# Kernel tuning notes

Hardware: AMD Instinct MI355X
Metric: run time of the kernel (lower is better)

## Reference

```python
import jax, jax.numpy as jnp
import numpy as np

N, D, E = 50000, 128, 100000
H1, H2, H3 = 8, 8, 4
NEG_SLOPE = 0.2  # PyG GATv2Conv default negative_slope


def _gatv2_layer(x, src, dst, Wl, Wr, att, b, heads):
    # GATv2Conv(in=D, out=D, heads=heads, concat=False), share_weights=False
    C = Wl.shape[1] // heads
    xl = (x @ Wl).reshape(-1, heads, C)  # source-side transform (x_j)
    xr = (x @ Wr).reshape(-1, heads, C)  # target-side transform (x_i)
    m = jax.nn.leaky_relu(xl[src] + xr[dst], NEG_SLOPE)      # [E,H,C]
    e = jnp.einsum('ehc,hc->eh', m, att)                      # [E,H]
    # segment softmax over incoming edges of each destination node
    emax = jax.ops.segment_max(e, dst, num_segments=N)        # [N,H]
    a = jnp.exp(e - emax[dst])
    denom = jax.ops.segment_sum(a, dst, num_segments=N)       # [N,H] (>0: self-loops)
    a = a / denom[dst]
    out = jax.ops.segment_sum(xl[src] * a[:, :, None], dst, num_segments=N)  # [N,H,C]
    return out.mean(axis=1) + b  # concat=False -> head mean, then bias


def setup_inputs() -> dict:
    key = jax.random.key(0)
    ks = jax.random.split(key, 16)
    x = jax.random.normal(ks[0], (N, D), dtype=jnp.float32)
    src = jax.random.randint(ks[1], (E,), 0, N)
    dst = jax.random.randint(ks[2], (E,), 0, N)
    src = jnp.where(src == dst, (src + 1) % N, src)  # no pre-existing self loops
    edge_index = jnp.stack([src, dst]).astype(jnp.int64)
    s = 1.0 / np.sqrt(D)
    def lin(k, h):
        return jax.random.uniform(k, (D, h * D), jnp.float32, -s, s)
    def attn(k, h):
        return jax.random.uniform(k, (h, D), jnp.float32, -s, s)
    return {
        'x': x, 'edge_index': edge_index,
        'W1l': lin(ks[3], H1), 'W1r': lin(ks[4], H1), 'att1': attn(ks[5], H1), 'b1': jnp.zeros((D,), jnp.float32),
        'W2l': lin(ks[6], H2), 'W2r': lin(ks[7], H2), 'att2': attn(ks[8], H2), 'b2': jnp.zeros((D,), jnp.float32),
        'W3l': lin(ks[9], H3), 'W3r': lin(ks[10], H3), 'att3': attn(ks[11], H3), 'b3': jnp.zeros((D,), jnp.float32),
    }


def reference(x, edge_index, W1l, W1r, att1, b1, W2l, W2r, att2, b2, W3l, W3r, att3, b3):
    # PyG GATv2Conv adds self loops by default
    loops = jnp.arange(N, dtype=edge_index.dtype)
    src = jnp.concatenate([edge_index[0], loops])
    dst = jnp.concatenate([edge_index[1], loops])
    h = x + _gatv2_layer(x, src, dst, W1l, W1r, att1, b1, H1)
    h = jax.nn.elu(h)  # dropout is identity in eval mode
    h = h + _gatv2_layer(h, src, dst, W2l, W2r, att2, b2, H2)
    h = jax.nn.elu(h)
    h = h + _gatv2_layer(h, src, dst, W3l, W3r, att3, b3, H3)
    return h
```

## Files before the change

kernel.cpp:

```cpp
#include <hip/hip_runtime.h>

#define NN 50000
#define DD 128
#define EE 100000
#define ET (EE + NN)

typedef __attribute__((ext_vector_type(4))) float f32x4;
typedef __attribute__((ext_vector_type(8))) short bf16x8;
typedef __attribute__((ext_vector_type(4))) unsigned short u16x4;
typedef __attribute__((ext_vector_type(4))) unsigned int u32x4;
typedef __attribute__((ext_vector_type(2))) unsigned int u32x2;

static __device__ __forceinline__ unsigned short f2bf(float f) {
  union { float f; unsigned int u; } v; v.f = f;
  unsigned int r = (v.u + 0x7FFFu + ((v.u >> 16) & 1u)) >> 16;
  return (unsigned short)r;
}
static __device__ __forceinline__ float bflo(unsigned int u) {
  union { unsigned int u; float f; } v; v.u = u << 16; return v.f;
}
static __device__ __forceinline__ float bfhi(unsigned int u) {
  union { unsigned int u; float f; } v; v.u = u & 0xffff0000u; return v.f;
}

template <int CTRL>
static __device__ __forceinline__ float dpp_add(float x) {
  int xi = __builtin_bit_cast(int, x);
  int yi = __builtin_amdgcn_update_dpp(xi, xi, CTRL, 0xF, 0xF, true);
  return x + __builtin_bit_cast(float, yi);
}
static __device__ __forceinline__ float row16_sum(float p) {
  p = dpp_add<0xB1>(p);
  p = dpp_add<0x4E>(p);
  p = dpp_add<0x141>(p);
  p = dpp_add<0x128>(p);
  return p;
}

__global__ __launch_bounds__(256) void k_prep(
    const float* __restrict__ x, const int* __restrict__ ei,
    const float* __restrict__ W1l, const float* __restrict__ W1r,
    const float* __restrict__ W2l, const float* __restrict__ W2r,
    const float* __restrict__ W3l, const float* __restrict__ W3r,
    const float* __restrict__ att1, const float* __restrict__ att2, const float* __restrict__ att3,
    unsigned short* __restrict__ wt1, unsigned short* __restrict__ wt2,
    unsigned short* __restrict__ wt3,
    float* __restrict__ as1, float* __restrict__ as2, float* __restrict__ as3,
    unsigned short* __restrict__ abf, int* __restrict__ counts) {
  const int i = blockIdx.x * 256 + threadIdx.x;
  const float LOG2E = 1.4426950408889634f;
  if (i < 262144) {
    int half = i >> 17, rem = i & 131071;
    int nn = rem >> 7, k = rem & 127;
    const float* W = half ? W1r : W1l;
    wt1[i] = f2bf(W[(size_t)k * 1024 + nn]);
  } else if (i < 524288) {
    int local = i - 262144;
    int half = local >> 17, rem = local & 131071;
    int nn = rem >> 7, k = rem & 127;
    const float* W = half ? W2r : W2l;
    wt2[local] = f2bf(W[(size_t)k * 1024 + nn]);
  } else if (i < 655360) {
    int local = i - 524288;
    int half = local >> 16, rem = local & 65535;
    int nn = rem >> 7, k = rem & 127;
    const float* W = half ? W3r : W3l;
    wt3[local] = f2bf(W[(size_t)k * 512 + nn]);
  } else if (i < 657920) {
    int local = i - 655360;
    if (local < 1024) as1[local] = att1[local] * LOG2E;
    else if (local < 2048) as2[local - 1024] = att2[local - 1024] * LOG2E;
    else as3[local - 2048] = att3[local - 2048] * LOG2E;
  } else if (i < 807920) {
    int e = i - 657920;
    int dst = (e < EE) ? ei[EE + e] : (e - EE);
    if (dst >= 0 && dst < NN) atomicAdd(&counts[dst], 1);
  } else if (i < 2407920) {
    int u = i - 807920;
    f32x4 v = *(const f32x4*)(x + (size_t)u * 4);
    u16x4 w;
    w.x = f2bf(v.x); w.y = f2bf(v.y); w.z = f2bf(v.z); w.w = f2bf(v.w);
    *(u16x4*)(abf + (size_t)u * 4) = w;
  }
}

__global__ __launch_bounds__(1024) void k_scan(const int* __restrict__ counts,
                                               int* __restrict__ offs,
                                               int* __restrict__ cursor) {
  __shared__ int wsum[16];
  __shared__ int wpre[16];
  __shared__ int wtot;
  const int tid = threadIdx.x;
  const int wv = tid >> 6, lane = tid & 63;
  int carry = 0;
  for (int base = 0; base < NN; base += 4096) {
    int i0 = base + tid * 4;
    int v[4];
#pragma unroll
    for (int q = 0; q < 4; ++q) { int i = i0 + q; v[q] = (i < NN) ? counts[i] : 0; }
    int s = v[0] + v[1] + v[2] + v[3];
    int sc = s;
#pragma unroll
    for (int m = 1; m < 64; m <<= 1) {
      int t = __shfl_up(sc, m, 64);
      if (lane >= m) sc += t;
    }
    if (lane == 63) wsum[wv] = sc;
    __syncthreads();
    if (tid < 16) {
      int t = wsum[tid];
      int scc = t;
#pragma unroll
      for (int m = 1; m < 16; m <<= 1) {
        int u = __shfl_up(scc, m, 64);
        if (tid >= m) scc += u;
      }
      wpre[tid] = scc - t;
      if (tid == 15) wtot = scc;
    }
    __syncthreads();
    int excl = carry + wpre[wv] + (sc - s);
#pragma unroll
    for (int q = 0; q < 4; ++q) {
      int i = i0 + q;
      if (i < NN) { offs[i] = excl; cursor[i] = excl; }
      excl += v[q];
    }
    carry += wtot;
    __syncthreads();
  }
  if (tid == 0) offs[NN] = carry;
}

__global__ void k_fill(const int* __restrict__ ei, int* __restrict__ cursor,
                       int* __restrict__ srcs) {
  int i = blockIdx.x * blockDim.x + threadIdx.x;
  if (i >= ET) return;
  int src, dst;
  if (i < EE) { src = ei[i]; dst = ei[EE + i]; }
  else { src = dst = i - EE; }
  if (dst < 0 || dst >= NN) return;
  if (src < 0 || src >= NN) src = dst;
  int pos = atomicAdd(&cursor[dst], 1);
  if (pos >= 0 && pos < ET) srcs[pos] = src;
}

__global__ __launch_bounds__(256) void gemm_bt(
    const unsigned short* __restrict__ A, const unsigned short* __restrict__ WT,
    unsigned short* __restrict__ Cl, unsigned short* __restrict__ Cr,
    int M, int Nout, int lgny) {
  const int f = (blockIdx.x & 7) * (gridDim.x >> 3) + (blockIdx.x >> 3);
  const int c = f & ((1 << lgny) - 1);
  const int x = f >> lgny;
  const int z = c & 1, y = c >> 1;
  const int m0 = x * 128, n0 = y * 128;
  unsigned short* C = z ? Cr : Cl;
  const unsigned short* BT = WT + (size_t)z * Nout * DD;

  __shared__ unsigned short As[128 * 128];
  __shared__ unsigned short Bs[128 * 128];
  const int tid = threadIdx.x;
  const int wave = tid >> 6, lane = tid & 63;
  const int hi = lane >> 4, lr = lane & 15;

#pragma unroll
  for (int i = 0; i < 8; ++i) {
    int row = i * 16 + wave * 4 + hi;
    int c16 = lr ^ (row & 7);
    const unsigned short* ga = A + (size_t)(m0 + row) * DD + c16 * 8;
    __builtin_amdgcn_global_load_lds((const __attribute__((address_space(1))) void*)ga,
        (__attribute__((address_space(3))) void*)(As + i * 2048 + wave * 512), 16, 0, 0);
    const unsigned short* gb = BT + (size_t)(n0 + row) * DD + c16 * 8;
    __builtin_amdgcn_global_load_lds((const __attribute__((address_space(1))) void*)gb,
        (__attribute__((address_space(3))) void*)(Bs + i * 2048 + wave * 512), 16, 0, 0);
  }
  __syncthreads();

  const int wr = (wave >> 1) * 64, wc = (wave & 1) * 64;
  f32x4 acc[4][4];
#pragma unroll
  for (int i = 0; i < 4; ++i)
#pragma unroll
    for (int j = 0; j < 4; ++j) acc[i][j] = (f32x4){0.f, 0.f, 0.f, 0.f};

#pragma unroll
  for (int k0 = 0; k0 < 128; k0 += 32) {
    const int ck = (k0 >> 3) + hi;
    bf16x8 af[4], bfr[4];
#pragma unroll
    for (int mi = 0; mi < 4; ++mi) {
      int r = wr + mi * 16 + lr;
      af[mi] = *(const bf16x8*)&As[r * 128 + ((ck ^ (r & 7)) << 3)];
    }
#pragma unroll
    for (int ni = 0; ni < 4; ++ni) {
      int cc = wc + ni * 16 + lr;
      bfr[ni] = *(const bf16x8*)&Bs[cc * 128 + ((ck ^ (cc & 7)) << 3)];
    }
#pragma unroll
    for (int mi = 0; mi < 4; ++mi)
#pragma unroll
      for (int ni = 0; ni < 4; ++ni)
        acc[mi][ni] = __builtin_amdgcn_mfma_f32_16x16x32_bf16(af[mi], bfr[ni], acc[mi][ni], 0, 0, 0);
  }

#pragma unroll
  for (int mi = 0; mi < 4; ++mi) {
#pragma unroll
    for (int ni = 0; ni < 4; ++ni) {
      int col = n0 + wc + ni * 16 + lr;
#pragma unroll
      for (int j = 0; j < 4; ++j) {
        int row = m0 + wr + mi * 16 + (hi << 2) + j;
        if (row < M) C[(size_t)row * Nout + col] = f2bf(acc[mi][ni][j]);
      }
    }
  }
}

template <int H>
__global__ __launch_bounds__(256) void gat_agg8(
    const unsigned short* __restrict__ xl, const unsigned short* __restrict__ xr,
    const int* __restrict__ offs, const int* __restrict__ srcs,
    const float* __restrict__ att_s,
    const float* __restrict__ bias,
    const float* __restrict__ residf,
    const unsigned short* __restrict__ residb,
    float* __restrict__ outf,
    unsigned short* __restrict__ hbfw,
    int do_elu) {
  constexpr int HG = H / 2;
  constexpr int CPL = 2 * HG;
  constexpr int NW = HG;
  constexpr int LPH = 128 / CPL;
  constexpr int ROW = H * DD;
  constexpr int HALFROW = ROW / 2;
  const int wave = threadIdx.x >> 6, lane = threadIdx.x & 63;
  const int nsub = wave >> 1, g = wave & 1;
  const int n = blockIdx.x * 2 + nsub;
  if (n >= NN) return;
  const int cb = g * HALFROW + lane * CPL;
  const int d0 = (lane * CPL) & 127;

  float xrv[CPL], av[CPL];
  {
    unsigned int uw[NW];
    if constexpr (NW == 4) {
      u32x4 v = *(const u32x4*)(xr + (size_t)n * ROW + cb);
      uw[0] = v.x; uw[1] = v.y; uw[2] = v.z; uw[3] = v.w;
    } else {
      u32x2 v = *(const u32x2*)(xr + (size_t)n * ROW + cb);
      uw[0] = v.x; uw[1] = v.y;
    }
#pragma unroll
    for (int w = 0; w < NW; ++w) {
      xrv[2 * w] = bflo(uw[w]);
      xrv[2 * w + 1] = bfhi(uw[w]);
    }
#pragma unroll
    for (int c = 0; c < CPL; ++c) av[c] = att_s[cb + c];
  }

  float acc[CPL];
#pragma unroll
  for (int c = 0; c < CPL; ++c) acc[c] = 0.f;
  float mx = -1e30f, dn = 0.f;

  const int e0 = offs[n], e1 = offs[n + 1];
  const unsigned short* xl_cb = xl + cb;
  for (int j = e0; j < e1; j += 4) {
    const int B = (e1 - j < 4) ? (e1 - j) : 4;
    unsigned int rows[4][NW];
#pragma unroll
    for (int b = 0; b < 4; ++b) {
      if (b < B) {
        int s = srcs[j + b];
        if constexpr (NW == 4) {
          u32x4 v = *(const u32x4*)(xl_cb + (size_t)s * ROW);
          rows[b][0] = v.x; rows[b][1] = v.y; rows[b][2] = v.z; rows[b][3] = v.w;
        } else {
          u32x2 v = *(const u32x2*)(xl_cb + (size_t)s * ROW);
          rows[b][0] = v.x; rows[b][1] = v.y;
        }
      }
    }
    float p[4];
#pragma unroll
    for (int b = 0; b < 4; ++b) {
      float pp = -1e30f;
      if (b < B) {
        pp = 0.f;
#pragma unroll
        for (int w = 0; w < NW; ++w) {
          float x0 = bflo(rows[b][w]), x1 = bfhi(rows[b][w]);
          float z0 = x0 + xrv[2 * w]; z0 = fmaxf(z0, 0.2f * z0);
          float z1 = x1 + xrv[2 * w + 1]; z1 = fmaxf(z1, 0.2f * z1);
          pp = fmaf(z0, av[2 * w], pp);
          pp = fmaf(z1, av[2 * w + 1], pp);
        }
        pp = row16_sum(pp);
        if constexpr (LPH == 32) pp += __shfl_xor(pp, 16, 64);
      }
      p[b] = pp;
    }
    float pm = fmaxf(fmaxf(p[0], p[1]), fmaxf(p[2], p[3]));
    if (__any(pm > mx + 11.5f)) {
      float mnew = fmaxf(mx, pm);
      float sc = __builtin_amdgcn_exp2f(mx - mnew);
      dn *= sc;
#pragma unroll
      for (int c = 0; c < CPL; ++c) acc[c] *= sc;
      mx = mnew;
    }
#pragma unroll
    for (int b = 0; b < 4; ++b) {
      if (b < B) {
        float wt = __builtin_amdgcn_exp2f(p[b] - mx);
        dn += wt;
#pragma unroll
        for (int w = 0; w < NW; ++w) {
          acc[2 * w] = fmaf(wt, bflo(rows[b][w]), acc[2 * w]);
          acc[2 * w + 1] = fmaf(wt, bfhi(rows[b][w]), acc[2 * w + 1]);
        }
      }
    }
  }

  float r[CPL];
  const float inv = (1.f / (float)H) / dn;
#pragma unroll
  for (int c = 0; c < CPL; ++c) r[c] = acc[c] * inv;
#pragma unroll
  for (int m = LPH; m < 64; m <<= 1)
#pragma unroll
    for (int c = 0; c < CPL; ++c) r[c] += __shfl_xor(r[c], m, 64);

  __shared__ float lds[2][DD];
  if (g == 1 && lane < LPH) {
#pragma unroll
    for (int c = 0; c < CPL; ++c) lds[nsub][d0 + c] = r[c];
  }
  __syncthreads();
  if (g == 0 && lane < LPH) {
    float rv[CPL];
    if (residf) {
#pragma unroll
      for (int c = 0; c < CPL; c += 4) {
        f32x4 v = *(const f32x4*)(residf + (size_t)n * DD + d0 + c);
        rv[c] = v.x; rv[c + 1] = v.y; rv[c + 2] = v.z; rv[c + 3] = v.w;
      }
    } else {
      unsigned int uw[CPL / 2];
      if constexpr (CPL == 8) {
        u32x4 v = *(const u32x4*)(residb + (size_t)n * DD + d0);
        uw[0] = v.x; uw[1] = v.y; uw[2] = v.z; uw[3] = v.w;
      } else {
        u32x2 v = *(const u32x2*)(residb + (size_t)n * DD + d0);
        uw[0] = v.x; uw[1] = v.y;
      }
#pragma unroll
      for (int w = 0; w < CPL / 2; ++w) {
        rv[2 * w] = bflo(uw[w]);
        rv[2 * w + 1] = bfhi(uw[w]);
      }
    }
    float o[CPL];
#pragma unroll
    for (int c = 0; c < CPL; ++c) {
      o[c] = r[c] + lds[nsub][d0 + c] + bias[d0 + c] + rv[c];
      if (do_elu && o[c] < 0.f)
        o[c] = __builtin_amdgcn_exp2f(o[c] * 1.4426950408889634f) - 1.f;
    }
    if (outf) {
#pragma unroll
      for (int c = 0; c < CPL; c += 4) {
        f32x4 v; v.x = o[c]; v.y = o[c + 1]; v.z = o[c + 2]; v.w = o[c + 3];
        *(f32x4*)(outf + (size_t)n * DD + d0 + c) = v;
      }
    }
    if (hbfw) {
      unsigned int pk[CPL / 2];
#pragma unroll
      for (int q = 0; q < CPL / 2; ++q)
        pk[q] = (unsigned int)f2bf(o[2 * q]) | ((unsigned int)f2bf(o[2 * q + 1]) << 16);
      if constexpr (CPL == 8) {
        u32x4 v; v.x = pk[0]; v.y = pk[1]; v.z = pk[2]; v.w = pk[3];
        *(u32x4*)(hbfw + (size_t)n * DD + d0) = v;
      } else {
        u32x2 v; v.x = pk[0]; v.y = pk[1];
        *(u32x2*)(hbfw + (size_t)n * DD + d0) = v;
      }
    }
  }
}

extern "C" void kernel_launch(void* const* d_in, const int* in_sizes, int n_in,
                              void* d_out, int out_size, void* d_ws, size_t ws_size,
                              hipStream_t stream) {
  const float* x = (const float*)d_in[0];
  const int* ei = (const int*)d_in[1];
  const float* W1l = (const float*)d_in[2];
  const float* W1r = (const float*)d_in[3];
  const float* att1 = (const float*)d_in[4];
  const float* b1 = (const float*)d_in[5];
  const float* W2l = (const float*)d_in[6];
  const float* W2r = (const float*)d_in[7];
  const float* att2 = (const float*)d_in[8];
  const float* b2 = (const float*)d_in[9];
  const float* W3l = (const float*)d_in[10];
  const float* W3r = (const float*)d_in[11];
  const float* att3 = (const float*)d_in[12];
  const float* b3 = (const float*)d_in[13];
  float* out = (float*)d_out;

  char* p = (char*)d_ws;
  auto carve = [&](size_t bytes) {
    char* r = p;
    p += (bytes + 255) & ~(size_t)255;
    return r;
  };
  unsigned short* xl = (unsigned short*)carve((size_t)NN * 1024 * 2);
  unsigned short* xr = (unsigned short*)carve((size_t)NN * 1024 * 2);
  unsigned short* abf = (unsigned short*)carve((size_t)NN * DD * 2);
  unsigned short* wt1 = (unsigned short*)carve((size_t)2 * 1024 * DD * 2);
  unsigned short* wt2 = (unsigned short*)carve((size_t)2 * 1024 * DD * 2);
  unsigned short* wt3 = (unsigned short*)carve((size_t)2 * 512 * DD * 2);
  float* as1 = (float*)carve((size_t)8 * DD * 4);
  float* as2 = (float*)carve((size_t)8 * DD * 4);
  float* as3 = (float*)carve((size_t)4 * DD * 4);
  int* counts = (int*)carve((size_t)NN * 4);
  int* offs = (int*)carve(((size_t)NN + 1) * 4);
  int* cursor = (int*)carve((size_t)NN * 4);
  int* srcs = (int*)carve((size_t)ET * 4);
  size_t needed = (size_t)(p - (char*)d_ws);
  if (needed > ws_size) return;

  hipMemsetAsync(counts, 0, (size_t)NN * 4, stream);
  k_prep<<<9406, 256, 0, stream>>>(x, ei, W1l, W1r, W2l, W2r, W3l, W3r, att1, att2, att3,
                                   wt1, wt2, wt3, as1, as2, as3, abf, counts);
  k_scan<<<1, 1024, 0, stream>>>(counts, offs, cursor);
  k_fill<<<(ET + 255) / 256, 256, 0, stream>>>(ei, cursor, srcs);

  const int gx = (NN + 127) / 128;
  const int ga = (NN + 1) / 2;
  gemm_bt<<<gx * 16, 256, 0, stream>>>(abf, wt1, xl, xr, NN, 1024, 4);
  gat_agg8<8><<<ga, 256, 0, stream>>>(xl, xr, offs, srcs, as1, b1, x, nullptr,
                                      nullptr, abf, 1);
  gemm_bt<<<gx * 16, 256, 0, stream>>>(abf, wt2, xl, xr, NN, 1024, 4);
  gat_agg8<8><<<ga, 256, 0, stream>>>(xl, xr, offs, srcs, as2, b2, nullptr, abf,
                                      nullptr, abf, 1);
  gemm_bt<<<gx * 8, 256, 0, stream>>>(abf, wt3, xl, xr, NN, 512, 3);
  gat_agg8<4><<<ga, 256, 0, stream>>>(xl, xr, offs, srcs, as3, b3, nullptr, abf,
                                      out, nullptr, 0);
}
```

Baseline: 451.9 us.

## Shrink GEMM tiles to 64x64 and transpose weights via LDS-tiled kernel

Replaces the 128x128 bf16 MFMA GEMM tile with a 64x64 tile, launching more blocks with a quarter of the LDS each to improve occupancy and load balance. Moves the weight transpose/convert out of the elementwise prep kernel into a dedicated kernel that stages 64x64 tiles in shared memory for coalesced reads and writes. Smaller tiles reduce operand reuse, increasing global traffic for A and W.

```diff
diff --git a/kernel.cpp b/kernel.cpp
--- a/kernel.cpp
+++ b/kernel.cpp
@@ -37,46 +37,59 @@
   return p;
 }
 
-__global__ __launch_bounds__(256) void k_prep(
-    const float* __restrict__ x, const int* __restrict__ ei,
+__global__ __launch_bounds__(256) void k_wtr(
     const float* __restrict__ W1l, const float* __restrict__ W1r,
     const float* __restrict__ W2l, const float* __restrict__ W2r,
     const float* __restrict__ W3l, const float* __restrict__ W3r,
+    unsigned short* __restrict__ wt1, unsigned short* __restrict__ wt2,
+    unsigned short* __restrict__ wt3) {
+  __shared__ float t[64][65];
+  int b = blockIdx.x;
+  const float* W; unsigned short* WT; int Nout, lgn;
+  int half, tile;
+  if (b < 64) {
+    half = b >> 5; tile = b & 31; W = half ? W1r : W1l;
+    WT = wt1 + (size_t)half * 131072; Nout = 1024; lgn = 4;
+  } else if (b < 128) {
+    b -= 64; half = b >> 5; tile = b & 31; W = half ? W2r : W2l;
+    WT = wt2 + (size_t)half * 131072; Nout = 1024; lgn = 4;
+  } else {
+    b -= 128; half = b >> 4; tile = b & 15; W = half ? W3r : W3l;
+    WT = wt3 + (size_t)half * 65536; Nout = 512; lgn = 3;
+  }
+  const int k0 = (tile >> lgn) << 6;
+  const int n0 = (tile & ((1 << lgn) - 1)) << 6;
+  const int wv = threadIdx.x >> 6, ln = threadIdx.x & 63;
+#pragma unroll
+  for (int r = 0; r < 16; ++r) {
+    int row = r * 4 + wv;
+    t[row][ln] = W[(size_t)(k0 + row) * Nout + n0 + ln];
+  }
+  __syncthreads();
+#pragma unroll
+  for (int r = 0; r < 16; ++r) {
+    int nrow = r * 4 + wv;
+    WT[(size_t)(n0 + nrow) * 128 + k0 + ln] = f2bf(t[ln][nrow]);
+  }
+}
+
+__global__ __launch_bounds__(256) void k_prep(
+    const float* __restrict__ x, const int* __restrict__ ei,
     const float* __restrict__ att1, const float* __restrict__ att2, const float* __restrict__ att3,
-    unsigned short* __restrict__ wt1, unsigned short* __restrict__ wt2,
-    unsigned short* __restrict__ wt3,
     float* __restrict__ as1, float* __restrict__ as2, float* __restrict__ as3,
     unsigned short* __restrict__ abf, int* __restrict__ counts) {
   const int i = blockIdx.x * 256 + threadIdx.x;
   const float LOG2E = 1.4426950408889634f;
-  if (i < 262144) {
-    int half = i >> 17, rem = i & 131071;
-    int nn = rem >> 7, k = rem & 127;
-    const float* W = half ? W1r : W1l;
-    wt1[i] = f2bf(W[(size_t)k * 1024 + nn]);
-  } else if (i < 524288) {
-    int local = i - 262144;
-    int half = local >> 17, rem = local & 131071;
-    int nn = rem >> 7, k = rem & 127;
-    const float* W = half ? W2r : W2l;
-    wt2[local] = f2bf(W[(size_t)k * 1024 + nn]);
-  } else if (i < 655360) {
-    int local = i - 524288;
-    int half = local >> 16, rem = local & 65535;
-    int nn = rem >> 7, k = rem & 127;
-    const float* W = half ? W3r : W3l;
-    wt3[local] = f2bf(W[(size_t)k * 512 + nn]);
-  } else if (i < 657920) {
-    int local = i - 655360;
-    if (local < 1024) as1[local] = att1[local] * LOG2E;
-    else if (local < 2048) as2[local - 1024] = att2[local - 1024] * LOG2E;
-    else as3[local - 2048] = att3[local - 2048] * LOG2E;
-  } else if (i < 807920) {
-    int e = i - 657920;
+  if (i < 2560) {
+    if (i < 1024) as1[i] = att1[i] * LOG2E;
+    else if (i < 2048) as2[i - 1024] = att2[i - 1024] * LOG2E;
+    else as3[i - 2048] = att3[i - 2048] * LOG2E;
+  } else if (i < 152560) {
+    int e = i - 2560;
     int dst = (e < EE) ? ei[EE + e] : (e - EE);
     if (dst >= 0 && dst < NN) atomicAdd(&counts[dst], 1);
-  } else if (i < 2407920) {
-    int u = i - 807920;
+  } else if (i < 1752560) {
+    int u = i - 152560;
     f32x4 v = *(const f32x4*)(x + (size_t)u * 4);
     u16x4 w;
     w.x = f2bf(v.x); w.y = f2bf(v.y); w.z = f2bf(v.z); w.w = f2bf(v.w);
@@ -145,26 +158,26 @@
   if (pos >= 0 && pos < ET) srcs[pos] = src;
 }
 
-__global__ __launch_bounds__(256) void gemm_bt(
+__global__ __launch_bounds__(256) void gemm64(
     const unsigned short* __restrict__ A, const unsigned short* __restrict__ WT,
     unsigned short* __restrict__ Cl, unsigned short* __restrict__ Cr,
-    int M, int Nout, int lgny) {
+    int M, int Nout, int lgnc) {
   const int f = (blockIdx.x & 7) * (gridDim.x >> 3) + (blockIdx.x >> 3);
-  const int c = f & ((1 << lgny) - 1);
-  const int x = f >> lgny;
+  const int c = f & ((1 << lgnc) - 1);
+  const int x = f >> lgnc;
   const int z = c & 1, y = c >> 1;
-  const int m0 = x * 128, n0 = y * 128;
+  const int m0 = x * 64, n0 = y * 64;
   unsigned short* C = z ? Cr : Cl;
   const unsigned short* BT = WT + (size_t)z * Nout * DD;
 
-  __shared__ unsigned short As[128 * 128];
-  __shared__ unsigned short Bs[128 * 128];
+  __shared__ unsigned short As[64 * 128];
+  __shared__ unsigned short Bs[64 * 128];
   const int tid = threadIdx.x;
   const int wave = tid >> 6, lane = tid & 63;
   const int hi = lane >> 4, lr = lane & 15;
 
 #pragma unroll
-  for (int i = 0; i < 8; ++i) {
+  for (int i = 0; i < 4; ++i) {
     int row = i * 16 + wave * 4 + hi;
     int c16 = lr ^ (row & 7);
     const unsigned short* ga = A + (size_t)(m0 + row) * DD + c16 * 8;
@@ -176,38 +189,38 @@
   }
   __syncthreads();
 
-  const int wr = (wave >> 1) * 64, wc = (wave & 1) * 64;
-  f32x4 acc[4][4];
-#pragma unroll
-  for (int i = 0; i < 4; ++i)
-#pragma unroll
-    for (int j = 0; j < 4; ++j) acc[i][j] = (f32x4){0.f, 0.f, 0.f, 0.f};
+  const int wr = (wave >> 1) * 32, wc = (wave & 1) * 32;
+  f32x4 acc[2][2];
+#pragma unroll
+  for (int i = 0; i < 2; ++i)
+#pragma unroll
+    for (int j = 0; j < 2; ++j) acc[i][j] = (f32x4){0.f, 0.f, 0.f, 0.f};
 
 #pragma unroll
   for (int k0 = 0; k0 < 128; k0 += 32) {
     const int ck = (k0 >> 3) + hi;
-    bf16x8 af[4], bfr[4];
-#pragma unroll
-    for (int mi = 0; mi < 4; ++mi) {
+    bf16x8 af[2], bfr[2];
+#pragma unroll
+    for (int mi = 0; mi < 2; ++mi) {
       int r = wr + mi * 16 + lr;
       af[mi] = *(const bf16x8*)&As[r * 128 + ((ck ^ (r & 7)) << 3)];
     }
 #pragma unroll
-    for (int ni = 0; ni < 4; ++ni) {
+    for (int ni = 0; ni < 2; ++ni) {
       int cc = wc + ni * 16 + lr;
       bfr[ni] = *(const bf16x8*)&Bs[cc * 128 + ((ck ^ (cc & 7)) << 3)];
     }
 #pragma unroll
-    for (int mi = 0; mi < 4; ++mi)
-#pragma unroll
-      for (int ni = 0; ni < 4; ++ni)
+    for (int mi = 0; mi < 2; ++mi)
+#pragma unroll
+      for (int ni = 0; ni < 2; ++ni)
         acc[mi][ni] = __builtin_amdgcn_mfma_f32_16x16x32_bf16(af[mi], bfr[ni], acc[mi][ni], 0, 0, 0);
   }
 
 #pragma unroll
-  for (int mi = 0; mi < 4; ++mi) {
-#pragma unroll
-    for (int ni = 0; ni < 4; ++ni) {
+  for (int mi = 0; mi < 2; ++mi) {
+#pragma unroll
+    for (int ni = 0; ni < 2; ++ni) {
       int col = n0 + wc + ni * 16 + lr;
 #pragma unroll
       for (int j = 0; j < 4; ++j) {
@@ -436,20 +449,20 @@
   if (needed > ws_size) return;
 
   hipMemsetAsync(counts, 0, (size_t)NN * 4, stream);
-  k_prep<<<9406, 256, 0, stream>>>(x, ei, W1l, W1r, W2l, W2r, W3l, W3r, att1, att2, att3,
-                                   wt1, wt2, wt3, as1, as2, as3, abf, counts);
+  k_wtr<<<160, 256, 0, stream>>>(W1l, W1r, W2l, W2r, W3l, W3r, wt1, wt2, wt3);
+  k_prep<<<6847, 256, 0, stream>>>(x, ei, att1, att2, att3, as1, as2, as3, abf, counts);
   k_scan<<<1, 1024, 0, stream>>>(counts, offs, cursor);
   k_fill<<<(ET + 255) / 256, 256, 0, stream>>>(ei, cursor, srcs);
 
-  const int gx = (NN + 127) / 128;
+  const int gx = (NN + 63) / 64;
   const int ga = (NN + 1) / 2;
-  gemm_bt<<<gx * 16, 256, 0, stream>>>(abf, wt1, xl, xr, NN, 1024, 4);
+  gemm64<<<gx * 32, 256, 0, stream>>>(abf, wt1, xl, xr, NN, 1024, 5);
   gat_agg8<8><<<ga, 256, 0, stream>>>(xl, xr, offs, srcs, as1, b1, x, nullptr,
                                       nullptr, abf, 1);
-  gemm_bt<<<gx * 16, 256, 0, stream>>>(abf, wt2, xl, xr, NN, 1024, 4);
+  gemm64<<<gx * 32, 256, 0, stream>>>(abf, wt2, xl, xr, NN, 1024, 5);
   gat_agg8<8><<<ga, 256, 0, stream>>>(xl, xr, offs, srcs, as2, b2, nullptr, abf,
                                       nullptr, abf, 1);
-  gemm_bt<<<gx * 8, 256, 0, stream>>>(abf, wt3, xl, xr, NN, 512, 3);
+  gemm64<<<gx * 16, 256, 0, stream>>>(abf, wt3, xl, xr, NN, 512, 4);
   gat_agg8<4><<<ga, 256, 0, stream>>>(xl, xr, offs, srcs, as3, b3, nullptr, abf,
                                       out, nullptr, 0);
 }
```

New measurement: 449.6 us. About the same (-0.5%).
